# Kernel optimization log

Hardware: AMD Instinct MI355X
Metric: run time of the kernel (lower is better)

Reference implementation:

```python
import jax, jax.numpy as jnp
import numpy as np
import math

B, S, D, H = 2, 2048, 1024, 16

def setup_inputs() -> dict:
    key = jax.random.key(0)
    ks = jax.random.split(key, 13)
    def lin(kw, kb, out_d, in_d):
        W = jax.random.normal(kw, (out_d, in_d), dtype=jnp.float32) * 0.02
        b = jax.random.normal(kb, (out_d,), dtype=jnp.float32) * 0.02
        return W, b
    Wq, bq = lin(ks[0], ks[1], D, D)
    Wk, bk = lin(ks[2], ks[3], D, D)
    Wv, bv = lin(ks[4], ks[5], D, D)
    Wo, bo = lin(ks[6], ks[7], D, D)
    query = jax.random.normal(ks[8], (B, S, D), dtype=jnp.float32)
    key_t = jax.random.normal(ks[9], (B, S, D), dtype=jnp.float32)
    value = jax.random.normal(ks[10], (B, S, D), dtype=jnp.float32)
    src_mask = jax.random.randint(ks[11], (B, S), 0, 2).astype(bool)  # True = masked out
    return {"query": query, "key": key_t, "value": value, "src_mask": src_mask,
            "Wq": Wq, "bq": bq, "Wk": Wk, "bk": bk, "Wv": Wv, "bv": bv,
            "Wo": Wo, "bo": bo, "nhead": H}

def reference(query, key, value, src_mask, Wq, bq, Wk, bk, Wv, bv, Wo, bo, nhead):
    b, s, d = query.shape
    hd = d // nhead
    scale = 1.0 / math.sqrt(hd)
    def split_heads(x):  # [b,s,d] -> [b,h,s,hd]
        return x.reshape(b, -1, nhead, hd).transpose(0, 2, 1, 3)
    q = split_heads(query @ Wq.T + bq)
    k = split_heads(key @ Wk.T + bk)
    v = split_heads(value @ Wv.T + bv)
    scores = jnp.einsum('bhqe,bhke->bhqk', q, k) * scale  # [b,h,s,s]
    # mask True -> -9e9, broadcast over heads and query positions (matches repeat)
    scores = jnp.where(src_mask[:, None, None, :], jnp.float32(-9e9), scores)
    probs = jax.nn.softmax(scores, axis=-1)
    # dropout is identity in eval mode
    out = jnp.einsum('bhqk,bhke->bhqe', probs, v)  # [b,h,s,hd]
    out = out.transpose(0, 2, 1, 3).reshape(b, s, d)
    out = out @ Wo.T + bo
    return out
```

## Files before the change

### kernel.cpp

```cpp
#include <hip/hip_runtime.h>
#include <hip/hip_bf16.h>
#include <cstdint>
#include <cstddef>

#define B_ 2
#define S_ 2048
#define D_ 1024
#define H_ 16
#define HD_ 64
#define M_ 4096

typedef __attribute__((ext_vector_type(8))) short short8;
typedef __attribute__((ext_vector_type(4))) float floatx4;
typedef __attribute__((ext_vector_type(16))) float f32x16;
typedef __attribute__((ext_vector_type(2))) int intx2;

__device__ __forceinline__ floatx4 mfma32(short8 a, short8 b, floatx4 c) {
    return __builtin_amdgcn_mfma_f32_16x16x32_bf16(a, b, c, 0, 0, 0);
}
__device__ __forceinline__ f32x16 mfma3216(short8 a, short8 b, f32x16 c) {
    return __builtin_amdgcn_mfma_f32_32x32x16_bf16(a, b, c, 0, 0, 0);
}

__device__ __forceinline__ void gload_lds16(const __hip_bfloat16* g, __hip_bfloat16* lds_base) {
    __builtin_amdgcn_global_load_lds(
        (const __attribute__((address_space(1))) void*)g,
        (__attribute__((address_space(3))) void*)lds_base, 16, 0, 0);
}

__device__ __forceinline__ int pkbf(float a, float b) {
    union { __hip_bfloat162 h; int i; } u;
    u.h = __float22bfloat162_rn({a, b});
    return u.i;
}
__device__ __forceinline__ void pl32swap(int& a, int& b) {
    intx2 r = __builtin_amdgcn_permlane32_swap(a, b, false, false);
    a = r.x; b = r.y;
}

__global__ __launch_bounds__(256) void cvt_all_kernel(
    const float* __restrict__ q, const float* __restrict__ k, const float* __restrict__ v,
    const float* __restrict__ wq, const float* __restrict__ wk,
    const float* __restrict__ wv, const float* __restrict__ wo,
    const int* __restrict__ mask,
    __hip_bfloat16* __restrict__ dstIn,
    __hip_bfloat16* __restrict__ dstW,
    float* __restrict__ fbias)
{
    const int bid = blockIdx.x;
    const int tid = threadIdx.x;
    const size_t SZ_IN = (size_t)M_ * D_;
    const size_t SZ_W  = (size_t)D_ * D_;
    if (bid < 12288) {
        int z = bid >> 12, xb = bid & 4095;
        const float* src = z == 0 ? q : z == 1 ? k : v;
        __hip_bfloat16* d = dstIn + (size_t)z * SZ_IN;
        int i = (xb * 256 + tid) * 4;
        float4 val = *(const float4*)(src + i);
        union { __hip_bfloat16 h[4]; uint2 u; } cv;
        cv.h[0] = __float2bfloat16(val.x); cv.h[1] = __float2bfloat16(val.y);
        cv.h[2] = __float2bfloat16(val.z); cv.h[3] = __float2bfloat16(val.w);
        *(uint2*)(d + i) = cv.u;
    } else if (bid < 16384) {
        int r  = bid - 12288;
        int z  = r >> 10, xb = r & 1023;
        const float* src = z == 0 ? wq : z == 1 ? wk : z == 2 ? wv : wo;
        __hip_bfloat16* d = dstW + (size_t)z * SZ_W;
        int i = (xb * 256 + tid) * 4;
        float4 val = *(const float4*)(src + i);
        union { __hip_bfloat16 h[4]; uint2 u; } cv;
        cv.h[0] = __float2bfloat16(val.x); cv.h[1] = __float2bfloat16(val.y);
        cv.h[2] = __float2bfloat16(val.z); cv.h[3] = __float2bfloat16(val.w);
        *(uint2*)(d + i) = cv.u;
    } else {
        int i = ((bid - 16384) * 256 + tid) * 4;
        int4 m = *(const int4*)(mask + i);
        float4 o;
        o.x = m.x ? -100000.0f : 0.0f;
        o.y = m.y ? -100000.0f : 0.0f;
        o.z = m.z ? -100000.0f : 0.0f;
        o.w = m.w ? -100000.0f : 0.0f;
        *(float4*)(fbias + i) = o;
    }
}

template <int MODE>
__device__ __forceinline__ void gemm_core(
    const __hip_bfloat16* __restrict__ A,
    const __hip_bfloat16* __restrict__ W,
    const float* __restrict__ bias,
    void* __restrict__ Cout,
    __hip_bfloat16* __restrict__ smem,
    int m0, int n0, int N)
{
    __hip_bfloat16* As = smem;
    __hip_bfloat16* Bs = smem + 128 * 32;
    const int K = D_;
    const int tid  = threadIdx.x;
    const int wave = tid >> 6;
    const int lane = tid & 63;
    const int quad = lane >> 4;
    const int l15  = lane & 15;
    const int wm   = (wave & 1) * 64;
    const int wn   = (wave >> 1) * 64;
    const int srow = lane >> 2;
    const int scol = (lane & 3) * 8;

    floatx4 acc[4][4];
#pragma unroll
    for (int i = 0; i < 4; i++)
#pragma unroll
        for (int j = 0; j < 4; j++) {
            floatx4 z = {0.f, 0.f, 0.f, 0.f};
            acc[i][j] = z;
        }

    for (int k0 = 0; k0 < K; k0 += 32) {
        __syncthreads();
#pragma unroll
        for (int t = 0; t < 2; t++) {
            int r0 = wave * 32 + t * 16;
            gload_lds16(A + (size_t)(m0 + r0 + srow) * K + k0 + scol, As + r0 * 32);
            gload_lds16(W + (size_t)(n0 + r0 + srow) * K + k0 + scol, Bs + r0 * 32);
        }
        __syncthreads();

        short8 afr[4], bfr[4];
#pragma unroll
        for (int i = 0; i < 4; i++)
            afr[i] = *(const short8*)(As + (wm + i * 16 + l15) * 32 + quad * 8);
#pragma unroll
        for (int j = 0; j < 4; j++)
            bfr[j] = *(const short8*)(Bs + (wn + j * 16 + l15) * 32 + quad * 8);
#pragma unroll
        for (int i = 0; i < 4; i++)
#pragma unroll
            for (int j = 0; j < 4; j++)
                acc[i][j] = mfma32(afr[i], bfr[j], acc[i][j]);
    }

    if constexpr (MODE == 1) {
#pragma unroll
        for (int j = 0; j < 4; j++) {
            int col = n0 + wn + j * 16 + l15;
            int h = col >> 6, e = col & 63;
            float bv = bias[col];
#pragma unroll
            for (int i = 0; i < 4; i++) {
                int s0 = m0 + wm + i * 16 + quad * 4;
                int bb = s0 >> 11, sl = s0 & 2047;
                union { __hip_bfloat16 hx[4]; uint2 u; } pk;
#pragma unroll
                for (int r = 0; r < 4; r++)
                    pk.hx[r] = __float2bfloat16(acc[i][j][r] + bv);
                *(uint2*)((__hip_bfloat16*)Cout + (((size_t)bb * H_ + h) * HD_ + e) * S_ + sl) = pk.u;
            }
        }
    } else {
#pragma unroll
        for (int j = 0; j < 4; j++) {
            int col = n0 + wn + j * 16 + l15;
            float bv = bias[col];
#pragma unroll
            for (int i = 0; i < 4; i++) {
#pragma unroll
                for (int r = 0; r < 4; r++) {
                    int rowg = m0 + wm + i * 16 + quad * 4 + r;
                    ((__hip_bfloat16*)Cout)[(size_t)rowg * N + col] =
                        __float2bfloat16(acc[i][j][r] + bv);
                }
            }
        }
    }
}

__global__ __launch_bounds__(256) void qkv_gemm_kernel(
    const __hip_bfloat16* __restrict__ qb, const __hip_bfloat16* __restrict__ kb,
    const __hip_bfloat16* __restrict__ vb,
    const __hip_bfloat16* __restrict__ Wqb, const __hip_bfloat16* __restrict__ Wkb,
    const __hip_bfloat16* __restrict__ Wvb,
    const float* __restrict__ bq, const float* __restrict__ bk, const float* __restrict__ bv,
    __hip_bfloat16* __restrict__ Qp, __hip_bfloat16* __restrict__ Kp,
    __hip_bfloat16* __restrict__ Vt)
{
    __shared__ __hip_bfloat16 smem[2 * 128 * 32] __attribute__((aligned(16)));
    const int z = blockIdx.z;
    const __hip_bfloat16* A = z == 0 ? qb : z == 1 ? kb : vb;
    const __hip_bfloat16* W = z == 0 ? Wqb : z == 1 ? Wkb : Wvb;
    const float* bias = z == 0 ? bq : z == 1 ? bk : bv;
    int m0 = blockIdx.y * 128, n0 = blockIdx.x * 128;
    if (z < 2) gemm_core<0>(A, W, bias, z == 0 ? (void*)Qp : (void*)Kp, smem, m0, n0, D_);
    else       gemm_core<1>(A, W, bias, (void*)Vt, smem, m0, n0, D_);
}

__global__ __launch_bounds__(256) void oproj_gemm_kernel(
    const __hip_bfloat16* __restrict__ A, const __hip_bfloat16* __restrict__ W,
    const float* __restrict__ bias, float* __restrict__ out)
{
    __shared__ __hip_bfloat16 As[64 * 32]  __attribute__((aligned(16)));
    __shared__ __hip_bfloat16 Bs[128 * 32] __attribute__((aligned(16)));
    const int K = D_, N = D_;
    const int tid  = threadIdx.x;
    const int m0   = blockIdx.y * 64;
    const int n0   = blockIdx.x * 128;
    const int wave = tid >> 6;
    const int lane = tid & 63;
    const int quad = lane >> 4;
    const int l15  = lane & 15;
    const int wm   = (wave & 1) * 32;
    const int wn   = (wave >> 1) * 64;
    const int srow = lane >> 2;
    const int scol = (lane & 3) * 8;

    floatx4 acc[2][4];
#pragma unroll
    for (int i = 0; i < 2; i++)
#pragma unroll
        for (int j = 0; j < 4; j++) {
            floatx4 z = {0.f, 0.f, 0.f, 0.f};
            acc[i][j] = z;
        }

    for (int k0 = 0; k0 < K; k0 += 32) {
        __syncthreads();
        {
            int ra = wave * 16;
            gload_lds16(A + (size_t)(m0 + ra + srow) * K + k0 + scol, As + ra * 32);
#pragma unroll
            for (int t = 0; t < 2; t++) {
                int rb = wave * 32 + t * 16;
                gload_lds16(W + (size_t)(n0 + rb + srow) * K + k0 + scol, Bs + rb * 32);
            }
        }
        __syncthreads();

        short8 afr[2], bfr[4];
#pragma unroll
        for (int i = 0; i < 2; i++)
            afr[i] = *(const short8*)(As + (wm + i * 16 + l15) * 32 + quad * 8);
#pragma unroll
        for (int j = 0; j < 4; j++)
            bfr[j] = *(const short8*)(Bs + (wn + j * 16 + l15) * 32 + quad * 8);
#pragma unroll
        for (int i = 0; i < 2; i++)
#pragma unroll
            for (int j = 0; j < 4; j++)
                acc[i][j] = mfma32(afr[i], bfr[j], acc[i][j]);
    }

#pragma unroll
    for (int j = 0; j < 4; j++) {
        int col = n0 + wn + j * 16 + l15;
        float bv = bias[col];
#pragma unroll
        for (int i = 0; i < 2; i++) {
#pragma unroll
            for (int r = 0; r < 4; r++) {
                int rowg = m0 + wm + i * 16 + quad * 4 + r;
                out[(size_t)rowg * N + col] = acc[i][j][r] + bv;
            }
        }
    }
}

#define LDP 72
#define NTK (S_ / 64)
#define KVBUF (64 * LDP)
__global__ __launch_bounds__(512, 4) void flash_attn_kernel(
    const __hip_bfloat16* __restrict__ Q,
    const __hip_bfloat16* __restrict__ Kp,
    const __hip_bfloat16* __restrict__ Vt,
    const float* __restrict__ fbias,
    __hip_bfloat16* __restrict__ O)
{
    __shared__ __hip_bfloat16 smem[4 * KVBUF] __attribute__((aligned(16)));

    const int tid  = threadIdx.x;
    const int q0   = blockIdx.x * 128;
    const int bh   = blockIdx.y;
    const int b    = bh >> 4;
    const int h    = bh & 15;
    const int warp = tid >> 6;
    const int qw   = warp & 3;
    const int kvh  = warp >> 2;
    const int lane = tid & 63;
    const int l31  = lane & 31;
    const int hi   = lane >> 5;
    const float kSc = 0.18033688f;

    const size_t baseQ = ((size_t)b * S_ + q0) * D_ + (size_t)h * HD_;
#pragma unroll
    for (int c = tid; c < 1024; c += 512) {
        int row = c >> 3, kc = c & 7;
        *(uint4*)(smem + row * LDP + kc * 8) =
            *(const uint4*)(Q + baseQ + (size_t)row * D_ + kc * 8);
    }
    __syncthreads();
    short8 qb[4];
#pragma unroll
    for (int ks = 0; ks < 4; ks++)
        qb[ks] = *(const short8*)(smem + (qw * 32 + l31) * LDP + ks * 16 + hi * 8);
    __syncthreads();

    const float* brow = fbias + b * S_;
    const __hip_bfloat16* VtBase = Vt + (size_t)bh * HD_ * S_;
    const size_t baseKrow = (size_t)b * S_ * D_ + (size_t)h * HD_;

    const int r0  = tid >> 3;
    const int kc0 = (tid & 7) * 8;

    uint4 kreg, vreg;
    auto issue = [&](int kv0) {
        kreg = *(const uint4*)(Kp + baseKrow + (size_t)(kv0 + r0) * D_ + kc0);
        vreg = *(const uint4*)(VtBase + (size_t)r0 * S_ + kv0 + kc0);
    };
    auto commit = [&](int pb) {
        *(uint4*)(smem + pb * KVBUF + r0 * LDP + kc0) = kreg;
        *(uint4*)(smem + (2 + pb) * KVBUF + r0 * LDP + kc0) = vreg;
    };

    issue(0);
    commit(0);
    __syncthreads();

    float lsum = 0.f;
    f32x16 o_acc[2];
#pragma unroll
    for (int hdb = 0; hdb < 2; hdb++)
#pragma unroll
        for (int r = 0; r < 16; r++) o_acc[hdb][r] = 0.f;

    for (int t = 0; t < NTK; ++t) {
        if (t) __syncthreads();

        if (t + 1 < NTK) issue((t + 1) * 64);

        const __hip_bfloat16* Ks  = smem + (t & 1) * KVBUF;
        const __hip_bfloat16* Vts = smem + (2 + (t & 1)) * KVBUF;

        f32x16 z;
#pragma unroll
        for (int r = 0; r < 16; r++) z[r] = 0.f;
        __builtin_amdgcn_s_setprio(1);
#pragma unroll
        for (int ks = 0; ks < 4; ks++) {
            short8 ka = *(const short8*)(Ks + (kvh * 32 + l31) * LDP + ks * 16 + hi * 8);
            z = mfma3216(ka, qb[ks], z);
        }
        __builtin_amdgcn_s_setprio(0);

        short8 pa[2];
#pragma unroll
        for (int ksl = 0; ksl < 2; ksl++) {
            const float* bb = brow + t * 64 + kvh * 32 + ksl * 16 + hi * 4;
            floatx4 b0 = *(const floatx4*)(bb);
            floatx4 b1 = *(const floatx4*)(bb + 8);
            float p[8];
#pragma unroll
            for (int i = 0; i < 8; i++) {
                float bias = (i < 4) ? b0[i & 3] : b1[i & 3];
                p[i] = __builtin_amdgcn_exp2f(z[ksl * 8 + i] * kSc + bias);
            }
            lsum += ((p[0] + p[1]) + (p[2] + p[3])) + ((p[4] + p[5]) + (p[6] + p[7]));
            int w0 = pkbf(p[0], p[1]);
            int w2 = pkbf(p[4], p[5]);
            int w1 = pkbf(p[2], p[3]);
            int w3 = pkbf(p[6], p[7]);
            pl32swap(w0, w2);
            pl32swap(w1, w3);
            union { int w[4]; short8 s; } fr;
            fr.w[0] = w0; fr.w[1] = w1; fr.w[2] = w2; fr.w[3] = w3;
            pa[ksl] = fr.s;
        }

        __builtin_amdgcn_s_setprio(1);
#pragma unroll
        for (int hdb = 0; hdb < 2; hdb++)
#pragma unroll
            for (int ksl = 0; ksl < 2; ksl++) {
                short8 vb = *(const short8*)(Vts + (hdb * 32 + l31) * LDP +
                                             kvh * 32 + ksl * 16 + hi * 8);
                o_acc[hdb] = mfma3216(pa[ksl], vb, o_acc[hdb]);
            }
        __builtin_amdgcn_s_setprio(0);

        if (t + 1 < NTK) commit((t + 1) & 1);
    }

    __syncthreads();
    float* ored = (float*)smem;
    float* lred = (float*)smem + 8192;
    if (kvh == 1) {
#pragma unroll
        for (int hdb = 0; hdb < 2; hdb++)
#pragma unroll
            for (int r = 0; r < 16; r++)
                ored[(hdb * 16 + r) * 256 + qw * 64 + lane] = o_acc[hdb][r];
        lred[qw * 64 + lane] = lsum;
    }
    __syncthreads();
    if (kvh == 0) {
#pragma unroll
        for (int hdb = 0; hdb < 2; hdb++)
#pragma unroll
            for (int r = 0; r < 16; r++)
                o_acc[hdb][r] += ored[(hdb * 16 + r) * 256 + qw * 64 + lane];
        float ls = lsum + lred[qw * 64 + lane];
        ls += __shfl_xor(ls, 32);
        float inv = 1.0f / ls;

        const size_t baseO = ((size_t)b * S_ + q0 + qw * 32) * D_ + (size_t)h * HD_;
#pragma unroll
        for (int r = 0; r < 16; r++) {
            int crow = (r & 3) + 8 * (r >> 2) + 4 * hi;
            float iv = __shfl(inv, crow);
#pragma unroll
            for (int hdb = 0; hdb < 2; hdb++)
                O[baseO + (size_t)crow * D_ + hdb * 32 + l31] =
                    __float2bfloat16(o_acc[hdb][r] * iv);
        }
    }
}

extern "C" void kernel_launch(void* const* d_in, const int* in_sizes, int n_in,
                              void* d_out, int out_size, void* d_ws, size_t ws_size,
                              hipStream_t stream) {
    const float* query = (const float*)d_in[0];
    const float* key   = (const float*)d_in[1];
    const float* value = (const float*)d_in[2];
    const int*   mask  = (const int*)d_in[3];
    const float* Wq    = (const float*)d_in[4];
    const float* bq    = (const float*)d_in[5];
    const float* Wk    = (const float*)d_in[6];
    const float* bk    = (const float*)d_in[7];
    const float* Wv    = (const float*)d_in[8];
    const float* bv    = (const float*)d_in[9];
    const float* Wo    = (const float*)d_in[10];
    const float* bo    = (const float*)d_in[11];
    float* out = (float*)d_out;

    const size_t SZ_IN = (size_t)M_ * D_;
    const size_t SZ_W  = (size_t)D_ * D_;
    __hip_bfloat16* qb  = (__hip_bfloat16*)d_ws;
    __hip_bfloat16* kb  = qb  + SZ_IN;
    __hip_bfloat16* vb  = kb  + SZ_IN;
    __hip_bfloat16* Wqb = vb  + SZ_IN;
    __hip_bfloat16* Wkb = Wqb + SZ_W;
    __hip_bfloat16* Wvb = Wkb + SZ_W;
    __hip_bfloat16* Wob = Wvb + SZ_W;
    __hip_bfloat16* Qp  = Wob + SZ_W;
    __hip_bfloat16* Kp  = Qp  + SZ_IN;
    __hip_bfloat16* Vt  = Kp  + SZ_IN;
    float*          fb  = (float*)(Vt + SZ_IN);

    cvt_all_kernel<<<dim3(16388), 256, 0, stream>>>(
        query, key, value, Wq, Wk, Wv, Wo, mask, qb, Wqb, fb);

    qkv_gemm_kernel<<<dim3(D_ / 128, M_ / 128, 3), 256, 0, stream>>>(
        qb, kb, vb, Wqb, Wkb, Wvb, bq, bk, bv, Qp, Kp, Vt);

    flash_attn_kernel<<<dim3(S_ / 128, B_ * H_), 512, 0, stream>>>(Qp, Kp, Vt, fb, Qp);

    oproj_gemm_kernel<<<dim3(D_ / 128, M_ / 64), 256, 0, stream>>>(Qp, Wob, bo, out);
}
```

Baseline: 229.5 us.

## Software-pipeline PV MFMAs across KV tiles and remap block indices for locality

The flash attention loop now delays the P·V MFMAs of each tile into the next iteration, issuing them alongside the QK^T MFMAs. The goal is to overlap exp/softmax VALU work with matrix-core work, and the V fragments are loaded into registers before the LDS buffer is overwritten. All three kernels also remap the linear block index so that consecutive blocks are spread across tiles, aiming at better L2 or cache-channel locality on the multi-XCD GPU. The cost is extra VGPRs for the held P and V fragments, which may hurt occupancy under launch_bounds(512,4).

```diff
diff --git a/kernel.cpp b/kernel.cpp
--- a/kernel.cpp
+++ b/kernel.cpp
@@ -188,7 +188,9 @@
     const __hip_bfloat16* A = z == 0 ? qb : z == 1 ? kb : vb;
     const __hip_bfloat16* W = z == 0 ? Wqb : z == 1 ? Wkb : Wvb;
     const float* bias = z == 0 ? bq : z == 1 ? bk : bv;
-    int m0 = blockIdx.y * 128, n0 = blockIdx.x * 128;
+    int lin  = blockIdx.y * 8 + blockIdx.x;
+    int work = (lin & 7) * 32 + (lin >> 3);
+    int m0 = (work >> 3) * 128, n0 = (work & 7) * 128;
     if (z < 2) gemm_core<0>(A, W, bias, z == 0 ? (void*)Qp : (void*)Kp, smem, m0, n0, D_);
     else       gemm_core<1>(A, W, bias, (void*)Vt, smem, m0, n0, D_);
 }
@@ -201,8 +203,10 @@
     __shared__ __hip_bfloat16 Bs[128 * 32] __attribute__((aligned(16)));
     const int K = D_, N = D_;
     const int tid  = threadIdx.x;
-    const int m0   = blockIdx.y * 64;
-    const int n0   = blockIdx.x * 128;
+    int lin  = blockIdx.y * 8 + blockIdx.x;
+    int work = (lin & 7) * 64 + (lin >> 3);
+    const int m0   = (work >> 3) * 64;
+    const int n0   = (work & 7) * 128;
     const int wave = tid >> 6;
     const int lane = tid & 63;
     const int quad = lane >> 4;
@@ -276,8 +280,10 @@
     __shared__ __hip_bfloat16 smem[4 * KVBUF] __attribute__((aligned(16)));
 
     const int tid  = threadIdx.x;
-    const int q0   = blockIdx.x * 128;
-    const int bh   = blockIdx.y;
+    int lin  = blockIdx.y * 16 + blockIdx.x;
+    int work = (lin & 7) * 64 + (lin >> 3);
+    const int q0   = (work & 15) * 128;
+    const int bh   = work >> 4;
     const int b    = bh >> 4;
     const int h    = bh & 15;
     const int warp = tid >> 6;
@@ -330,6 +336,9 @@
 #pragma unroll
         for (int r = 0; r < 16; r++) o_acc[hdb][r] = 0.f;
 
+    short8 pa_p[2];
+    short8 vfr_p[4];
+
     for (int t = 0; t < NTK; ++t) {
         if (t) __syncthreads();
 
@@ -347,9 +356,15 @@
             short8 ka = *(const short8*)(Ks + (kvh * 32 + l31) * LDP + ks * 16 + hi * 8);
             z = mfma3216(ka, qb[ks], z);
         }
+        if (t) {
+#pragma unroll
+            for (int hdb = 0; hdb < 2; hdb++)
+#pragma unroll
+                for (int ksl = 0; ksl < 2; ksl++)
+                    o_acc[hdb] = mfma3216(pa_p[ksl], vfr_p[hdb * 2 + ksl], o_acc[hdb]);
+        }
         __builtin_amdgcn_s_setprio(0);
 
-        short8 pa[2];
 #pragma unroll
         for (int ksl = 0; ksl < 2; ksl++) {
             const float* bb = brow + t * 64 + kvh * 32 + ksl * 16 + hi * 4;
@@ -370,22 +385,26 @@
             pl32swap(w1, w3);
             union { int w[4]; short8 s; } fr;
             fr.w[0] = w0; fr.w[1] = w1; fr.w[2] = w2; fr.w[3] = w3;
-            pa[ksl] = fr.s;
-        }
-
-        __builtin_amdgcn_s_setprio(1);
+            pa_p[ksl] = fr.s;
+        }
+
 #pragma unroll
         for (int hdb = 0; hdb < 2; hdb++)
 #pragma unroll
-            for (int ksl = 0; ksl < 2; ksl++) {
-                short8 vb = *(const short8*)(Vts + (hdb * 32 + l31) * LDP +
-                                             kvh * 32 + ksl * 16 + hi * 8);
-                o_acc[hdb] = mfma3216(pa[ksl], vb, o_acc[hdb]);
-            }
-        __builtin_amdgcn_s_setprio(0);
+            for (int ksl = 0; ksl < 2; ksl++)
+                vfr_p[hdb * 2 + ksl] = *(const short8*)(Vts + (hdb * 32 + l31) * LDP +
+                                                        kvh * 32 + ksl * 16 + hi * 8);
 
         if (t + 1 < NTK) commit((t + 1) & 1);
     }
+
+    __builtin_amdgcn_s_setprio(1);
+#pragma unroll
+    for (int hdb = 0; hdb < 2; hdb++)
+#pragma unroll
+        for (int ksl = 0; ksl < 2; ksl++)
+            o_acc[hdb] = mfma3216(pa_p[ksl], vfr_p[hdb * 2 + ksl], o_acc[hdb]);
+    __builtin_amdgcn_s_setprio(0);
 
     __syncthreads();
     float* ored = (float*)smem;
```

After: 221.7 us. 3.4% less time.
